# Kernel tuning notes

Hardware: AMD Instinct MI355X
Metric: run time of the kernel (lower is better)

## Reference

```python
import jax, jax.numpy as jnp
import numpy as np

B, M, N = 32, 512, 128
HH, WW = 128, 128

def setup_inputs() -> dict:
    key = jax.random.key(0)
    kx, kl = jax.random.split(key)
    x = jax.random.normal(kx, (B, M, N), dtype=jnp.float32)
    # non-overlapping locations per batch (module requires no overlap):
    # take first M entries of a random permutation of the H*W flat grid
    keys = jax.random.split(kl, B)
    flat = jax.vmap(lambda k: jax.random.permutation(k, HH * WW)[:M])(keys)  # (B, M)
    location = jnp.stack([flat // WW, flat % WW], axis=-1).astype(jnp.int64)  # (B, M, 2) as (y, x)
    return {"x": x, "location": location, "H": HH, "W": WW}

def reference(x, location, H, W):
    Bb, Mm, Nn = x.shape
    flat_idx = location[..., 0] * W + location[..., 1]          # (B, M)
    out = jnp.zeros((Bb, H * W, Nn), dtype=x.dtype)
    out = out.at[jnp.arange(Bb)[:, None], flat_idx].set(x)       # scatter all B*M entities at once
    return out.transpose(0, 2, 1).reshape(Bb, Nn, H, W)          # (B, N, H, W)
```

## Files before the change

### kernel.cpp

```cpp
#include <hip/hip_runtime.h>

constexpr int B  = 32;
constexpr int M  = 512;
constexpr int N  = 128;
constexpr int H  = 128;
constexpr int W  = 128;
constexpr int HW = H * W;

typedef float f4 __attribute__((ext_vector_type(4)));
typedef int   i4 __attribute__((ext_vector_type(4)));

__global__ __launch_bounds__(256)
void fused_scatter_kernel(const float* __restrict__ x,
                          const int* __restrict__ loc,
                          float* __restrict__ out) {
    __shared__ int lmap[1024];

    const int tid = threadIdx.x;
    const int bid = blockIdx.x;
    const int b  = bid >> 6;
    const int nh = (bid >> 4) & 3;
    const int pc = bid & 15;
    const int n0 = nh << 5;
    const int p0 = pc << 10;

    const i4 lv = *reinterpret_cast<const i4*>(loc + (b << 10) + (tid << 2));

    i4 neg = {-1, -1, -1, -1};
    *reinterpret_cast<i4*>(&lmap[tid << 2]) = neg;
    __syncthreads();

    const int f0 = (lv[0] << 7) + lv[1] - p0;
    const int f1 = (lv[2] << 7) + lv[3] - p0;
    if ((unsigned)f0 < 1024u) lmap[f0] = (tid << 1);
    if ((unsigned)f1 < 1024u) lmap[f1] = (tid << 1) + 1;
    __syncthreads();

    const i4 iv = *reinterpret_cast<const i4*>(&lmap[tid << 2]);
    const bool v0 = iv[0] >= 0, v1 = iv[1] >= 0, v2 = iv[2] >= 0, v3 = iv[3] >= 0;

    const float* xb = x + (b << 16) + n0;
    const float* a0 = xb + ((v0 ? iv[0] : 0) << 7);
    const float* a1 = xb + ((v1 ? iv[1] : 0) << 7);
    const float* a2 = xb + ((v2 ? iv[2] : 0) << 7);
    const float* a3 = xb + ((v3 ? iv[3] : 0) << 7);

    float* ob = out + (b << 21) + (n0 << 14) + p0 + (tid << 2);

    #pragma unroll
    for (int g = 0; g < 4; ++g) {
        f4 xv[2][4];
        #pragma unroll
        for (int q = 0; q < 2; ++q) {
            const int off = (g << 3) + (q << 2);
            xv[q][0] = *reinterpret_cast<const f4*>(a0 + off);
            xv[q][1] = *reinterpret_cast<const f4*>(a1 + off);
            xv[q][2] = *reinterpret_cast<const f4*>(a2 + off);
            xv[q][3] = *reinterpret_cast<const f4*>(a3 + off);
        }
        #pragma unroll
        for (int q = 0; q < 2; ++q) {
            float* o = ob + (((g << 3) + (q << 2)) << 14);
            #pragma unroll
            for (int j = 0; j < 4; ++j) {
                f4 v = {v0 ? xv[q][0][j] : 0.f,
                        v1 ? xv[q][1][j] : 0.f,
                        v2 ? xv[q][2][j] : 0.f,
                        v3 ? xv[q][3][j] : 0.f};
                *reinterpret_cast<f4*>(o + (j << 14)) = v;
            }
        }
    }
}

extern "C" void kernel_launch(void* const* d_in, const int* in_sizes, int n_in,
                              void* d_out, int out_size, void* d_ws, size_t ws_size,
                              hipStream_t stream) {
    const float* x   = (const float*)d_in[0];
    const int*   loc = (const int*)d_in[1];
    float* out = (float*)d_out;

    fused_scatter_kernel<<<2048, 256, 0, stream>>>(x, loc, out);
}
```

Before: 49.03 us.

## Compact threads by occupancy so all-empty quads store zeros without gathers

Each block now classifies its 256 threads by whether their 4-pixel quad contains any scattered entity. Using wave ballots and shared atomics, it builds a permutation so valid quads are handled by the leading threads and empty quads by trailing ones. Warps with only empty quads then issue zero stores and skip the gather loads and selects, which cuts divergence and wasted x reads. The cost is an extra barrier, the ballot and atomic work, and scattered output addresses for the permuted threads. The launch bounds also gain a minimum-blocks hint.

```diff
diff --git a/kernel.cpp b/kernel.cpp
--- a/kernel.cpp
+++ b/kernel.cpp
@@ -10,11 +10,13 @@
 typedef float f4 __attribute__((ext_vector_type(4)));
 typedef int   i4 __attribute__((ext_vector_type(4)));
 
-__global__ __launch_bounds__(256)
+__global__ __launch_bounds__(256, 4)
 void fused_scatter_kernel(const float* __restrict__ x,
                           const int* __restrict__ loc,
                           float* __restrict__ out) {
     __shared__ int lmap[1024];
+    __shared__ int qlist[256];
+    __shared__ int cnts[2];
 
     const int tid = threadIdx.x;
     const int bid = blockIdx.x;
@@ -28,6 +30,7 @@
 
     i4 neg = {-1, -1, -1, -1};
     *reinterpret_cast<i4*>(&lmap[tid << 2]) = neg;
+    if (tid < 2) cnts[tid] = 0;
     __syncthreads();
 
     const int f0 = (lv[0] << 7) + lv[1] - p0;
@@ -36,38 +39,71 @@
     if ((unsigned)f1 < 1024u) lmap[f1] = (tid << 1) + 1;
     __syncthreads();
 
-    const i4 iv = *reinterpret_cast<const i4*>(&lmap[tid << 2]);
-    const bool v0 = iv[0] >= 0, v1 = iv[1] >= 0, v2 = iv[2] >= 0, v3 = iv[3] >= 0;
+    const i4 mv = *reinterpret_cast<const i4*>(&lmap[tid << 2]);
+    const bool valid = (mv[0] >= 0) | (mv[1] >= 0) | (mv[2] >= 0) | (mv[3] >= 0);
 
-    const float* xb = x + (b << 16) + n0;
-    const float* a0 = xb + ((v0 ? iv[0] : 0) << 7);
-    const float* a1 = xb + ((v1 ? iv[1] : 0) << 7);
-    const float* a2 = xb + ((v2 ? iv[2] : 0) << 7);
-    const float* a3 = xb + ((v3 ? iv[3] : 0) << 7);
+    const int lane = tid & 63;
+    const unsigned long long mask  = __ballot(valid);
+    const unsigned long long below = (lane == 0) ? 0ull : (~0ull >> (64 - lane));
+    const int nv_wave = __popcll(mask);
 
-    float* ob = out + (b << 21) + (n0 << 14) + p0 + (tid << 2);
+    int baseV = 0, baseI = 0;
+    if (lane == 0) {
+        baseV = atomicAdd(&cnts[0], nv_wave);
+        baseI = atomicAdd(&cnts[1], 64 - nv_wave);
+    }
+    baseV = __shfl(baseV, 0);
+    baseI = __shfl(baseI, 0);
 
-    #pragma unroll
-    for (int g = 0; g < 4; ++g) {
-        f4 xv[2][4];
+    int slot;
+    if (valid) slot = baseV + __popcll(mask & below);
+    else       slot = 255 - (baseI + __popcll(~mask & below));
+    qlist[slot] = tid;
+    __syncthreads();
+
+    const int nvalid = cnts[0];
+
+    const int q  = qlist[tid];
+    const int pq = q << 2;
+    float* ob = out + (b << 21) + (n0 << 14) + p0 + pq;
+
+    if (tid >= nvalid) {
+        const f4 z = {0.f, 0.f, 0.f, 0.f};
         #pragma unroll
-        for (int q = 0; q < 2; ++q) {
-            const int off = (g << 3) + (q << 2);
-            xv[q][0] = *reinterpret_cast<const f4*>(a0 + off);
-            xv[q][1] = *reinterpret_cast<const f4*>(a1 + off);
-            xv[q][2] = *reinterpret_cast<const f4*>(a2 + off);
-            xv[q][3] = *reinterpret_cast<const f4*>(a3 + off);
-        }
+        for (int c = 0; c < 32; ++c)
+            *reinterpret_cast<f4*>(ob + (c << 14)) = z;
+    } else {
+        const i4 iv = *reinterpret_cast<const i4*>(&lmap[pq]);
+        const bool v0 = iv[0] >= 0, v1 = iv[1] >= 0, v2 = iv[2] >= 0, v3 = iv[3] >= 0;
+
+        const float* xb = x + (b << 16) + n0;
+        const float* a0 = xb + ((v0 ? iv[0] : 0) << 7);
+        const float* a1 = xb + ((v1 ? iv[1] : 0) << 7);
+        const float* a2 = xb + ((v2 ? iv[2] : 0) << 7);
+        const float* a3 = xb + ((v3 ? iv[3] : 0) << 7);
+
         #pragma unroll
-        for (int q = 0; q < 2; ++q) {
-            float* o = ob + (((g << 3) + (q << 2)) << 14);
+        for (int g = 0; g < 4; ++g) {
+            f4 xv[2][4];
             #pragma unroll
-            for (int j = 0; j < 4; ++j) {
-                f4 v = {v0 ? xv[q][0][j] : 0.f,
-                        v1 ? xv[q][1][j] : 0.f,
-                        v2 ? xv[q][2][j] : 0.f,
-                        v3 ? xv[q][3][j] : 0.f};
-                *reinterpret_cast<f4*>(o + (j << 14)) = v;
+            for (int u = 0; u < 2; ++u) {
+                const int off = (g << 3) + (u << 2);
+                xv[u][0] = *reinterpret_cast<const f4*>(a0 + off);
+                xv[u][1] = *reinterpret_cast<const f4*>(a1 + off);
+                xv[u][2] = *reinterpret_cast<const f4*>(a2 + off);
+                xv[u][3] = *reinterpret_cast<const f4*>(a3 + off);
+            }
+            #pragma unroll
+            for (int u = 0; u < 2; ++u) {
+                float* o = ob + (((g << 3) + (u << 2)) << 14);
+                #pragma unroll
+                for (int j = 0; j < 4; ++j) {
+                    f4 v = {v0 ? xv[u][0][j] : 0.f,
+                            v1 ? xv[u][1][j] : 0.f,
+                            v2 ? xv[u][2][j] : 0.f,
+                            v3 ? xv[u][3][j] : 0.f};
+                    *reinterpret_cast<f4*>(o + (j << 14)) = v;
+                }
             }
         }
     }
```

Result: slower. 60.81 us (+24.0%).
